# Optimization experiments

Measured on AMD Instinct MI355X. Metric: run time of the kernel, lower is better.

The kernel has to match this reference:

```python
import jax, jax.numpy as jnp
import numpy as np

N_NODES = 50000
IN_C, HID, N_CLS = 128, 128, 16
N_EDGES = 800000


def gcn_conv(x, W, b, src, dst, deg_inv_sqrt, n_nodes):
    # PyG GCNConv: h = x @ W; out[dst] += norm * h[src]; out += b
    h = x @ W                                   # [N, out_c]
    norm = deg_inv_sqrt[src] * deg_inv_sqrt[dst]  # [E]
    msgs = h[src] * norm[:, None]               # gather + scale, [E, out_c]
    out = jax.ops.segment_sum(msgs, dst, num_segments=n_nodes)
    return out + b


def setup_inputs() -> dict:
    key = jax.random.key(0)
    k1, k2, k3, k4, k5 = jax.random.split(key, 5)
    x = jax.random.normal(k1, (N_NODES, IN_C), dtype=jnp.float32)
    edge_index = jax.random.randint(k2, (2, N_EDGES), 0, N_NODES, dtype=jnp.int64)
    # glorot-ish params (torch.manual_seed(1234) in source only affects init values)
    def lin(k, fan_in, fan_out):
        s = 1.0 / np.sqrt(fan_in)
        kw, kb = jax.random.split(k)
        W = jax.random.uniform(kw, (fan_in, fan_out), minval=-s, maxval=s, dtype=jnp.float32)
        b = jax.random.uniform(kb, (fan_out,), minval=-s, maxval=s, dtype=jnp.float32)
        return W, b
    W1, b1 = lin(k3, IN_C, HID)
    W2, b2 = lin(k4, HID, HID)
    Wh, bh = lin(k5, HID, N_CLS)
    return {"x": x, "edge_index": edge_index, "W1": W1, "b1": b1,
            "W2": W2, "b2": b2, "Wh": Wh, "bh": bh}


def reference(x, edge_index, W1, b1, W2, b2, Wh, bh):
    n = x.shape[0]
    # add self-loops (PyG GCNConv default add_self_loops=True)
    loops = jnp.arange(n, dtype=edge_index.dtype)
    src = jnp.concatenate([edge_index[0], loops])
    dst = jnp.concatenate([edge_index[1], loops])
    # symmetric normalization D^{-1/2} (A+I) D^{-1/2}; degree over dst with unit weights
    deg = jax.ops.segment_sum(jnp.ones(src.shape[0], dtype=x.dtype), dst, num_segments=n)
    dis = jnp.where(deg > 0, jax.lax.rsqrt(deg), 0.0)
    h = gcn_conv(x, W1, b1, src, dst, dis, n)
    h = jax.nn.relu(h)
    h = gcn_conv(h, W2, b2, src, dst, dis, n)
    h = jax.nn.relu(h)
    return h @ Wh + bh
```

## Files before the change

### kernel.cpp

```cpp
#include <hip/hip_runtime.h>

#define CH 128
#define NCLS 16
#define CHK 16
#define NCHUNK 8
#define ECAP 131072

typedef __attribute__((ext_vector_type(8))) short bf16x8;
typedef __attribute__((ext_vector_type(4))) float f32x4;

__device__ inline ushort f2bf(float f) {
    unsigned u = __float_as_uint(f);
    unsigned r = u + 0x7fffu + ((u >> 16) & 1u);
    return (ushort)(r >> 16);
}
__device__ inline float bf2f(ushort b) {
    return __uint_as_float(((unsigned)b) << 16);
}

__global__ __launch_bounds__(256) void prep_kernel(
    const float* __restrict__ W1, const float* __restrict__ W2,
    ushort* __restrict__ w1hi, ushort* __restrict__ w1lo,
    ushort* __restrict__ w2hi, ushort* __restrict__ w2lo,
    int* __restrict__ cnt, int* __restrict__ pcnt, int* __restrict__ galloc,
    float* __restrict__ bufA, int n, int nbz) {
    int b = blockIdx.x, tid = threadIdx.x;
    if (b < 128) {
        const float* W = (b < 64) ? W1 : W2;
        ushort* Whi = (b < 64) ? w1hi : w2hi;
        ushort* Wlo = (b < 64) ? w1lo : w2lo;
        int t = ((b & 63) << 8) + tid;
        int k = t >> 7, nn = t & 127;
        float v = W[t];
        ushort h = f2bf(v);
        Whi[nn * CH + k] = h;
        Wlo[nn * CH + k] = f2bf(v - bf2f(h));
    } else if (b < 128 + nbz) {
        int i = (b - 128) * 256 + tid;
        if (i < n) cnt[i] = 0;
    } else {
        if (tid < NCHUNK * CHK) {
            int c = tid >> 4, ch = tid & 15;
            bufA[((size_t)c * (n + 1) + n) * CHK + ch] = 0.0f;
        }
        if (tid < 8) pcnt[tid] = 0;
        if (tid == 8) *galloc = 0;
    }
}

__global__ __launch_bounds__(256) void bucketcount_kernel(
    const int* __restrict__ src, const int* __restrict__ dst,
    unsigned* __restrict__ ebuf, int* __restrict__ pcnt,
    int* __restrict__ cnt, int E, float p8n) {
    __shared__ int lpos[8];
    __shared__ int lbase[8];
    int tid = threadIdx.x;
    if (tid < 8) lpos[tid] = 0;
    __syncthreads();
    int i0 = (blockIdx.x * 256 + tid) * 4;
    int part[4]; int off[4]; unsigned pk[4]; int c = 0;
    if (i0 + 3 < E) {
        int4 s4 = *(const int4*)&src[i0];
        int4 d4 = *(const int4*)&dst[i0];
        int ss[4] = {s4.x, s4.y, s4.z, s4.w};
        int dd[4] = {d4.x, d4.y, d4.z, d4.w};
        c = 4;
#pragma unroll
        for (int k = 0; k < 4; k++) {
            part[k] = min(7, (int)((float)dd[k] * p8n));
            pk[k] = ((unsigned)dd[k] << 16) | (unsigned)ss[k];
            off[k] = atomicAdd(&lpos[part[k]], 1);
            atomicAdd(&cnt[dd[k]], 1);
        }
    } else {
        for (int k = 0; k < 4 && i0 + k < E; k++) {
            int s = src[i0 + k], d = dst[i0 + k];
            part[c] = min(7, (int)((float)d * p8n));
            pk[c] = ((unsigned)d << 16) | (unsigned)s;
            off[c] = atomicAdd(&lpos[part[c]], 1);
            atomicAdd(&cnt[d], 1);
            c++;
        }
    }
    __syncthreads();
    if (tid < 8) lbase[tid] = atomicAdd(&pcnt[tid], lpos[tid]);
    __syncthreads();
    for (int k = 0; k < c; k++) {
        int idx = lbase[part[k]] + off[k];
        if (idx < ECAP) ebuf[(size_t)part[k] * ECAP + idx] = pk[k];
    }
}

__global__ __launch_bounds__(256) void place_kernel(
    const int* __restrict__ cnt, int* __restrict__ rsp,
    int* __restrict__ cursor, int* __restrict__ galloc,
    ushort* __restrict__ esrc, int n) {
    __shared__ int lds[256];
    __shared__ int gbase;
    int t = threadIdx.x;
    int i = blockIdx.x * 256 + t;
    int c = (i < n) ? cnt[i] : 0;
    int sz = (i < n) ? ((c + 8) & ~7) : 0;
    lds[t] = sz;
    __syncthreads();
    for (int off = 1; off < 256; off <<= 1) {
        int x = (t >= off) ? lds[t - off] : 0;
        __syncthreads();
        lds[t] += x;
        __syncthreads();
    }
    int incl = lds[t];
    if (t == 255) gbase = atomicAdd(galloc, incl);
    __syncthreads();
    int base = gbase + incl - sz;
    if (i < n) {
        rsp[i] = base;
        cursor[i] = base + 1;
        esrc[base] = (ushort)i;
        for (int p = base + 1 + c; p < base + sz; p++) esrc[p] = (ushort)n;
    }
}

template <bool RELU_IN>
__device__ __forceinline__ void gemm_body(
    int bx, int by, const float* __restrict__ A,
    const ushort* __restrict__ Bthi, const ushort* __restrict__ Btlo,
    const int* __restrict__ cntp, float* __restrict__ C, int n_rows) {
    const int tid = threadIdx.x;
    const int bm0 = bx * 128;
    const int wv = tid >> 6;
    const int lane = tid & 63;
    const int col = lane & 15;
    const int quad = lane >> 4;
    const int rbase = bm0 + wv * 32 + col;
    const int ntBase = by * 4;

    f32x4 acc[2][4];
#pragma unroll
    for (int m = 0; m < 2; m++)
#pragma unroll
        for (int t = 0; t < 4; t++) acc[m][t] = (f32x4){0.f, 0.f, 0.f, 0.f};

#pragma unroll
    for (int k0 = 0; k0 < 4; k0++) {
        const int kb = k0 * 32 + quad * 8;
        bf16x8 ah[2], al[2];
#pragma unroll
        for (int m = 0; m < 2; m++) {
            int arow = rbase + m * 16;
            bool av = (arow < n_rows);
            const float* __restrict__ Ap = A + (size_t)arow * CH + kb;
            float4 f0 = av ? *(const float4*)Ap       : make_float4(0.f, 0.f, 0.f, 0.f);
            float4 f1 = av ? *(const float4*)(Ap + 4) : make_float4(0.f, 0.f, 0.f, 0.f);
            if (RELU_IN) {
                f0.x = fmaxf(f0.x, 0.f); f0.y = fmaxf(f0.y, 0.f);
                f0.z = fmaxf(f0.z, 0.f); f0.w = fmaxf(f0.w, 0.f);
                f1.x = fmaxf(f1.x, 0.f); f1.y = fmaxf(f1.y, 0.f);
                f1.z = fmaxf(f1.z, 0.f); f1.w = fmaxf(f1.w, 0.f);
            }
            float fa[8] = {f0.x, f0.y, f0.z, f0.w, f1.x, f1.y, f1.z, f1.w};
#pragma unroll
            for (int j = 0; j < 8; j++) {
                ushort h = f2bf(fa[j]);
                ah[m][j] = (short)h;
                al[m][j] = (short)f2bf(fa[j] - bf2f(h));
            }
        }
#pragma unroll
        for (int t = 0; t < 4; t++) {
            const int boff = ((ntBase + t) * 16 + col) * CH + kb;
            bf16x8 bh = *(const bf16x8*)&Bthi[boff];
            bf16x8 bl = *(const bf16x8*)&Btlo[boff];
#pragma unroll
            for (int m = 0; m < 2; m++) {
                acc[m][t] = __builtin_amdgcn_mfma_f32_16x16x32_bf16(ah[m], bh, acc[m][t], 0, 0, 0);
                acc[m][t] = __builtin_amdgcn_mfma_f32_16x16x32_bf16(ah[m], bl, acc[m][t], 0, 0, 0);
                acc[m][t] = __builtin_amdgcn_mfma_f32_16x16x32_bf16(al[m], bh, acc[m][t], 0, 0, 0);
            }
        }
    }

#pragma unroll
    for (int m = 0; m < 2; m++) {
#pragma unroll
        for (int reg = 0; reg < 4; reg++) {
            int gr = bm0 + wv * 32 + m * 16 + quad * 4 + reg;
            if (gr < n_rows) {
                float d = rsqrtf((float)cntp[gr] + 1.0f);
#pragma unroll
                for (int t = 0; t < 4; t++) {
                    int nt = ntBase + t;
                    __builtin_nontemporal_store(
                        acc[m][t][reg] * d,
                        &C[((size_t)nt * (n_rows + 1) + gr) * CHK + col]);
                }
            }
        }
    }
}

template <bool RELU_IN>
__global__ __launch_bounds__(256, 4) void gemmfill_kernel(
    const float* __restrict__ A, const ushort* __restrict__ Bthi,
    const ushort* __restrict__ Btlo, const int* __restrict__ cntp,
    float* __restrict__ C, int n_rows, int nbx, int gemmBlocks,
    const unsigned* __restrict__ ebuf, const int* __restrict__ pcnt,
    int* __restrict__ cursor, ushort* __restrict__ esrc) {
    int b = blockIdx.x;
    if (b < gemmBlocks) {
        gemm_body<RELU_IN>(b % nbx, b / nbx, A, Bthi, Btlo, cntp, C, n_rows);
    } else {
        int fb = b - gemmBlocks;
        int part = fb & 7;
        int m = min(pcnt[part], ECAP);
        const unsigned* bk = ebuf + (size_t)part * ECAP;
        for (int e = (fb >> 3) * 256 + (int)threadIdx.x; e < m; e += 256 * 256) {
            unsigned pe = bk[e];
            int p = atomicAdd(&cursor[pe >> 16], 1);
            esrc[p] = (ushort)(pe & 0xffffu);
        }
    }
}

__global__ __launch_bounds__(256) void gather_kernel(
    const int* __restrict__ rsp, const int* __restrict__ cnt,
    const ushort* __restrict__ esrc, const float* __restrict__ hC,
    const float* __restrict__ bias, float* __restrict__ out, int n) {
    int c = blockIdx.x & 7;
    int wv = threadIdx.x >> 6;
    int lane = threadIdx.x & 63;
    int g = lane >> 2;
    int q = lane & 3;
    int i = (blockIdx.x >> 3) * 64 + wv * 16 + g;
    bool valid = (i < n);
    int iw = valid ? i : 0;
    const float4* __restrict__ h4 = (const float4*)(hC + (size_t)c * (n + 1) * CHK);

    float warm = 0.f;
    {
        int nblk = (n + 63) >> 6;
        size_t p = (size_t)(blockIdx.x >> 3) * 256 + threadIdx.x;
        size_t sliceF4 = ((size_t)(n + 1) * CHK) >> 2;
        for (; p < sliceF4; p += (size_t)nblk * 256) {
            float4 v = h4[p];
            warm += v.x + v.y + v.z + v.w;
        }
    }

    int beg = valid ? rsp[iw] : 0;
    int cv  = valid ? cnt[iw] : -8;
    int pc  = (cv + 8) & ~7;
    float4 acc = make_float4(0.f, 0.f, 0.f, 0.f);
    for (int j = beg; j < beg + pc; j += 8) {
        ushort4 e0 = *(const ushort4*)&esrc[j];
        ushort4 e1 = *(const ushort4*)&esrc[j + 4];
        float4 v0 = h4[(size_t)e0.x * 4 + q];
        float4 v1 = h4[(size_t)e0.y * 4 + q];
        float4 v2 = h4[(size_t)e0.z * 4 + q];
        float4 v3 = h4[(size_t)e0.w * 4 + q];
        float4 v4 = h4[(size_t)e1.x * 4 + q];
        float4 v5 = h4[(size_t)e1.y * 4 + q];
        float4 v6 = h4[(size_t)e1.z * 4 + q];
        float4 v7 = h4[(size_t)e1.w * 4 + q];
        acc.x += v0.x; acc.y += v0.y; acc.z += v0.z; acc.w += v0.w;
        acc.x += v1.x; acc.y += v1.y; acc.z += v1.z; acc.w += v1.w;
        acc.x += v2.x; acc.y += v2.y; acc.z += v2.z; acc.w += v2.w;
        acc.x += v3.x; acc.y += v3.y; acc.z += v3.z; acc.w += v3.w;
        acc.x += v4.x; acc.y += v4.y; acc.z += v4.z; acc.w += v4.w;
        acc.x += v5.x; acc.y += v5.y; acc.z += v5.z; acc.w += v5.w;
        acc.x += v6.x; acc.y += v6.y; acc.z += v6.z; acc.w += v6.w;
        acc.x += v7.x; acc.y += v7.y; acc.z += v7.z; acc.w += v7.w;
    }
    __asm__ volatile("" : : "v"(warm));
    if (valid) {
        float di = rsqrtf((float)cv + 1.0f);
        float4 bv = ((const float4*)bias)[c * 4 + q];
        f32x4 o;
        o[0] = bv.x + di * acc.x;
        o[1] = bv.y + di * acc.y;
        o[2] = bv.z + di * acc.z;
        o[3] = bv.w + di * acc.w;
        __builtin_nontemporal_store(o, (f32x4*)&((float4*)out)[(size_t)iw * 32 + c * 4 + q]);
    }
}

__global__ __launch_bounds__(256) void head_kernel(
    const float* __restrict__ A, const float* __restrict__ Wh,
    const float* __restrict__ bh, float* __restrict__ out, int n) {
    __shared__ float Ws[CH * NCLS];
    __shared__ float As[16][129];
    const int tid = threadIdx.x;
    const int n0 = blockIdx.x * 16;
#pragma unroll
    for (int i = 0; i < 8; i++) {
        int l = tid + i * 256;
        Ws[l] = Wh[l];
    }
#pragma unroll
    for (int i = 0; i < 8; i++) {
        int l = tid + i * 256;
        int r = l >> 7, c = l & 127;
        int gr = n0 + r;
        As[r][c] = (gr < n) ? fmaxf(A[(size_t)gr * CH + c], 0.0f) : 0.0f;
    }
    __syncthreads();
    int r = tid >> 4, c = tid & 15;
    float acc = bh[c];
#pragma unroll
    for (int k = 0; k < CH; k++) acc = fmaf(As[r][k], Ws[k * NCLS + c], acc);
    int gr = n0 + r;
    if (gr < n) out[(size_t)gr * NCLS + c] = acc;
}

extern "C" void kernel_launch(void* const* d_in, const int* in_sizes, int n_in,
                              void* d_out, int out_size, void* d_ws, size_t ws_size,
                              hipStream_t stream) {
    const float* x  = (const float*)d_in[0];
    const int*   ei = (const int*)d_in[1];
    const float* W1 = (const float*)d_in[2];
    const float* b1 = (const float*)d_in[3];
    const float* W2 = (const float*)d_in[4];
    const float* b2 = (const float*)d_in[5];
    const float* Wh = (const float*)d_in[6];
    const float* bh = (const float*)d_in[7];
    float* out = (float*)d_out;

    const int n = in_sizes[0] / CH;
    const int E = in_sizes[1] / 2;
    const int* src = ei;
    const int* dst = ei + E;

    ushort* w1hi = (ushort*)d_ws;
    ushort* w1lo = w1hi + CH * CH;
    ushort* w2hi = w1lo + CH * CH;
    ushort* w2lo = w2hi + CH * CH;
    float* bufA = (float*)(w2lo + CH * CH);
    float* bufB = bufA + (size_t)(n + 1) * CH;
    int* cnt    = (int*)(bufB + (size_t)n * CH);
    int* rsp    = cnt + n;
    int* cursor = rsp + n;
    int* pcnt   = cursor + n;
    int* galloc = pcnt + 8;
    ushort* esrc = (ushort*)(pcnt + 16);
    unsigned* ebuf = (unsigned*)bufB;

    const int B = 256;
    const int nbz = (n + B - 1) / B;
    const int nbx = (n + 127) / 128;
    const int gemmBlocks = nbx * 2;
    const float p8n = 8.0f / (float)n;

    prep_kernel<<<128 + nbz + 1, B, 0, stream>>>(W1, W2, w1hi, w1lo, w2hi, w2lo,
                                                 cnt, pcnt, galloc, bufA, n, nbz);
    bucketcount_kernel<<<(E + 1023) / 1024, B, 0, stream>>>(src, dst, ebuf, pcnt,
                                                            cnt, E, p8n);
    place_kernel<<<nbz, B, 0, stream>>>(cnt, rsp, cursor, galloc, esrc, n);

    const int gatherGrid = NCHUNK * ((n + 63) / 64);

    gemmfill_kernel<false><<<gemmBlocks + 2048, B, 0, stream>>>(
        x, w1hi, w1lo, cnt, bufA, n, nbx, gemmBlocks, ebuf, pcnt, cursor, esrc);
    gather_kernel<<<gatherGrid, B, 0, stream>>>(rsp, cnt, esrc, bufA, b1, bufB, n);
    gemmfill_kernel<true><<<gemmBlocks, B, 0, stream>>>(
        bufB, w2hi, w2lo, cnt, bufA, n, nbx, gemmBlocks, ebuf, pcnt, cursor, esrc);
    gather_kernel<<<gatherGrid, B, 0, stream>>>(rsp, cnt, esrc, bufA, b2, bufB, n);
    head_kernel<<<(n + 15) / 16, B, 0, stream>>>(bufB, Wh, bh, out, n);
}
```

Before: 296.4 us.

## Sort nodes by degree bin within blocks to balance gather wavefront work

The place kernel now counting-sorts the 256 nodes of each block into 16 bins by padded edge count, and writes a per-block permutation. Gather threads then process nodes in that permuted order, so nodes with similar degree share a wavefront and lanes diverge less in the edge loop. The cost is an extra LDS histogram pass in place, one more indirection load in gather, and scattered output writes.

```diff
diff --git a/kernel.cpp b/kernel.cpp
--- a/kernel.cpp
+++ b/kernel.cpp
@@ -94,26 +94,41 @@
 __global__ __launch_bounds__(256) void place_kernel(
     const int* __restrict__ cnt, int* __restrict__ rsp,
     int* __restrict__ cursor, int* __restrict__ galloc,
-    ushort* __restrict__ esrc, int n) {
-    __shared__ int lds[256];
+    ushort* __restrict__ esrc, int* __restrict__ perm, int n) {
+    __shared__ int hist[16];
+    __shared__ int histBase[16];
+    __shared__ int scanArr[256];
     __shared__ int gbase;
     int t = threadIdx.x;
     int i = blockIdx.x * 256 + t;
-    int c = (i < n) ? cnt[i] : 0;
-    int sz = (i < n) ? ((c + 8) & ~7) : 0;
-    lds[t] = sz;
+    bool valid = (i < n);
+    int c = valid ? cnt[i] : 0;
+    int sz = valid ? ((c + 8) & ~7) : 0;
+    int k = valid ? min(sz >> 3, 15) : 15;
+    if (t < 16) hist[t] = 0;
+    __syncthreads();
+    int idxInBin = atomicAdd(&hist[k], 1);
+    __syncthreads();
+    if (t == 0) {
+        int s = 0;
+#pragma unroll
+        for (int b = 0; b < 16; b++) { histBase[b] = s; s += hist[b]; }
+    }
+    __syncthreads();
+    int r = histBase[k] + idxInBin;
+    scanArr[r] = sz;
     __syncthreads();
     for (int off = 1; off < 256; off <<= 1) {
-        int x = (t >= off) ? lds[t - off] : 0;
+        int x = (t >= off) ? scanArr[t - off] : 0;
         __syncthreads();
-        lds[t] += x;
+        scanArr[t] += x;
         __syncthreads();
     }
-    int incl = lds[t];
-    if (t == 255) gbase = atomicAdd(galloc, incl);
-    __syncthreads();
-    int base = gbase + incl - sz;
-    if (i < n) {
+    if (t == 255) gbase = atomicAdd(galloc, scanArr[255]);
+    __syncthreads();
+    int base = gbase + scanArr[r] - sz;
+    perm[blockIdx.x * 256 + r] = valid ? i : n;
+    if (valid) {
         rsp[i] = base;
         cursor[i] = base + 1;
         esrc[base] = (ushort)i;
@@ -224,16 +239,18 @@
 
 __global__ __launch_bounds__(256) void gather_kernel(
     const int* __restrict__ rsp, const int* __restrict__ cnt,
-    const ushort* __restrict__ esrc, const float* __restrict__ hC,
-    const float* __restrict__ bias, float* __restrict__ out, int n) {
+    const int* __restrict__ perm, const ushort* __restrict__ esrc,
+    const float* __restrict__ hC, const float* __restrict__ bias,
+    float* __restrict__ out, int n) {
     int c = blockIdx.x & 7;
     int wv = threadIdx.x >> 6;
     int lane = threadIdx.x & 63;
     int g = lane >> 2;
     int q = lane & 3;
-    int i = (blockIdx.x >> 3) * 64 + wv * 16 + g;
-    bool valid = (i < n);
-    int iw = valid ? i : 0;
+    int slot = (blockIdx.x >> 3) * 64 + wv * 16 + g;
+    int node = perm[slot];
+    bool valid = (node < n);
+    int iw = valid ? node : 0;
     const float4* __restrict__ h4 = (const float4*)(hC + (size_t)c * (n + 1) * CHK);
 
     float warm = 0.f;
@@ -341,11 +358,12 @@
     int* cursor = rsp + n;
     int* pcnt   = cursor + n;
     int* galloc = pcnt + 8;
-    ushort* esrc = (ushort*)(pcnt + 16);
+    int* perm   = galloc + 8;
+    const int nbz = (n + 255) / 256;
+    ushort* esrc = (ushort*)(perm + nbz * 256);
     unsigned* ebuf = (unsigned*)bufB;
 
     const int B = 256;
-    const int nbz = (n + B - 1) / B;
     const int nbx = (n + 127) / 128;
     const int gemmBlocks = nbx * 2;
     const float p8n = 8.0f / (float)n;
@@ -354,15 +372,15 @@
                                                  cnt, pcnt, galloc, bufA, n, nbz);
     bucketcount_kernel<<<(E + 1023) / 1024, B, 0, stream>>>(src, dst, ebuf, pcnt,
                                                             cnt, E, p8n);
-    place_kernel<<<nbz, B, 0, stream>>>(cnt, rsp, cursor, galloc, esrc, n);
+    place_kernel<<<nbz, B, 0, stream>>>(cnt, rsp, cursor, galloc, esrc, perm, n);
 
     const int gatherGrid = NCHUNK * ((n + 63) / 64);
 
     gemmfill_kernel<false><<<gemmBlocks + 2048, B, 0, stream>>>(
         x, w1hi, w1lo, cnt, bufA, n, nbx, gemmBlocks, ebuf, pcnt, cursor, esrc);
-    gather_kernel<<<gatherGrid, B, 0, stream>>>(rsp, cnt, esrc, bufA, b1, bufB, n);
+    gather_kernel<<<gatherGrid, B, 0, stream>>>(rsp, cnt, perm, esrc, bufA, b1, bufB, n);
     gemmfill_kernel<true><<<gemmBlocks, B, 0, stream>>>(
         bufB, w2hi, w2lo, cnt, bufA, n, nbx, gemmBlocks, ebuf, pcnt, cursor, esrc);
-    gather_kernel<<<gatherGrid, B, 0, stream>>>(rsp, cnt, esrc, bufA, b2, bufB, n);
+    gather_kernel<<<gatherGrid, B, 0, stream>>>(rsp, cnt, perm, esrc, bufA, b2, bufB, n);
     head_kernel<<<(n + 15) / 16, B, 0, stream>>>(bufB, Wh, bh, out, n);
 }
```

Result: slower. 305.4 us (+3.0%).

## Stage A tile through double-buffered LDS with coalesced loads and one-time bf16 split

Applied to the files above, without the earlier changes.

The GEMM now loads each 128-row A tile cooperatively with coalesced float4 reads, converts it to hi/lo bf16 once, and stores it into a double-buffered LDS tile padded to avoid bank conflicts. The MFMA loop then reads fragments from LDS while the next k-slice is prefetched from global memory. The intent is to improve global-load coalescing and overlap loads with MFMA work. In exchange it adds barriers and about 40KB of LDS per block, and lowers the launch-bounds occupancy hint from 4 to 3 blocks.

```diff
diff --git a/kernel.cpp b/kernel.cpp
--- a/kernel.cpp
+++ b/kernel.cpp
@@ -5,6 +5,7 @@
 #define CHK 16
 #define NCHUNK 8
 #define ECAP 131072
+#define LDSK 40
 
 typedef __attribute__((ext_vector_type(8))) short bf16x8;
 typedef __attribute__((ext_vector_type(4))) float f32x4;
@@ -125,50 +126,76 @@
 __device__ __forceinline__ void gemm_body(
     int bx, int by, const float* __restrict__ A,
     const ushort* __restrict__ Bthi, const ushort* __restrict__ Btlo,
-    const int* __restrict__ cntp, float* __restrict__ C, int n_rows) {
+    const int* __restrict__ cntp, float* __restrict__ C, int n_rows,
+    ushort (*Ahi)[128 * LDSK], ushort (*Alo)[128 * LDSK]) {
     const int tid = threadIdx.x;
     const int bm0 = bx * 128;
     const int wv = tid >> 6;
     const int lane = tid & 63;
     const int col = lane & 15;
     const int quad = lane >> 4;
-    const int rbase = bm0 + wv * 32 + col;
     const int ntBase = by * 4;
 
+    int srow[4], skk[4]; bool sval[4]; const float* sptr[4];
+#pragma unroll
+    for (int i = 0; i < 4; i++) {
+        int f4 = tid + i * 256;
+        srow[i] = f4 >> 3;
+        skk[i] = (f4 & 7) * 4;
+        sval[i] = (bm0 + srow[i]) < n_rows;
+        sptr[i] = A + (size_t)(bm0 + srow[i]) * CH + skk[i];
+    }
+
     f32x4 acc[2][4];
 #pragma unroll
     for (int m = 0; m < 2; m++)
 #pragma unroll
         for (int t = 0; t < 4; t++) acc[m][t] = (f32x4){0.f, 0.f, 0.f, 0.f};
 
+    float4 ld[4];
+    auto cvtStore = [&](int bsel) {
+#pragma unroll
+        for (int i = 0; i < 4; i++) {
+            float fv[4] = {ld[i].x, ld[i].y, ld[i].z, ld[i].w};
+            ushort hs[4], ls[4];
+#pragma unroll
+            for (int j = 0; j < 4; j++) {
+                float v = RELU_IN ? fmaxf(fv[j], 0.f) : fv[j];
+                ushort h = f2bf(v);
+                hs[j] = h;
+                ls[j] = f2bf(v - bf2f(h));
+            }
+            int o = srow[i] * LDSK + skk[i];
+            *(ushort4*)&Ahi[bsel][o] = make_ushort4(hs[0], hs[1], hs[2], hs[3]);
+            *(ushort4*)&Alo[bsel][o] = make_ushort4(ls[0], ls[1], ls[2], ls[3]);
+        }
+    };
+
+#pragma unroll
+    for (int i = 0; i < 4; i++)
+        ld[i] = sval[i] ? *(const float4*)(sptr[i]) : make_float4(0.f, 0.f, 0.f, 0.f);
+    cvtStore(0);
+    __syncthreads();
+
 #pragma unroll
     for (int k0 = 0; k0 < 4; k0++) {
-        const int kb = k0 * 32 + quad * 8;
+        if (k0 < 3) {
+#pragma unroll
+            for (int i = 0; i < 4; i++)
+                ld[i] = sval[i] ? *(const float4*)(sptr[i] + (k0 + 1) * 32)
+                                : make_float4(0.f, 0.f, 0.f, 0.f);
+        }
+        const int bsel = k0 & 1;
         bf16x8 ah[2], al[2];
 #pragma unroll
         for (int m = 0; m < 2; m++) {
-            int arow = rbase + m * 16;
-            bool av = (arow < n_rows);
-            const float* __restrict__ Ap = A + (size_t)arow * CH + kb;
-            float4 f0 = av ? *(const float4*)Ap       : make_float4(0.f, 0.f, 0.f, 0.f);
-            float4 f1 = av ? *(const float4*)(Ap + 4) : make_float4(0.f, 0.f, 0.f, 0.f);
-            if (RELU_IN) {
-                f0.x = fmaxf(f0.x, 0.f); f0.y = fmaxf(f0.y, 0.f);
-                f0.z = fmaxf(f0.z, 0.f); f0.w = fmaxf(f0.w, 0.f);
-                f1.x = fmaxf(f1.x, 0.f); f1.y = fmaxf(f1.y, 0.f);
-                f1.z = fmaxf(f1.z, 0.f); f1.w = fmaxf(f1.w, 0.f);
-            }
-            float fa[8] = {f0.x, f0.y, f0.z, f0.w, f1.x, f1.y, f1.z, f1.w};
-#pragma unroll
-            for (int j = 0; j < 8; j++) {
-                ushort h = f2bf(fa[j]);
-                ah[m][j] = (short)h;
-                al[m][j] = (short)f2bf(fa[j] - bf2f(h));
-            }
+            int o = (wv * 32 + m * 16 + col) * LDSK + quad * 8;
+            ah[m] = *(bf16x8*)&Ahi[bsel][o];
+            al[m] = *(bf16x8*)&Alo[bsel][o];
         }
 #pragma unroll
         for (int t = 0; t < 4; t++) {
-            const int boff = ((ntBase + t) * 16 + col) * CH + kb;
+            const int boff = ((ntBase + t) * 16 + col) * CH + k0 * 32 + quad * 8;
             bf16x8 bh = *(const bf16x8*)&Bthi[boff];
             bf16x8 bl = *(const bf16x8*)&Btlo[boff];
 #pragma unroll
@@ -178,6 +205,8 @@
                 acc[m][t] = __builtin_amdgcn_mfma_f32_16x16x32_bf16(al[m], bh, acc[m][t], 0, 0, 0);
             }
         }
+        if (k0 < 3) cvtStore((k0 + 1) & 1);
+        __syncthreads();
     }
 
 #pragma unroll
@@ -200,15 +229,18 @@
 }
 
 template <bool RELU_IN>
-__global__ __launch_bounds__(256, 4) void gemmfill_kernel(
+__global__ __launch_bounds__(256, 3) void gemmfill_kernel(
     const float* __restrict__ A, const ushort* __restrict__ Bthi,
     const ushort* __restrict__ Btlo, const int* __restrict__ cntp,
     float* __restrict__ C, int n_rows, int nbx, int gemmBlocks,
     const unsigned* __restrict__ ebuf, const int* __restrict__ pcnt,
     int* __restrict__ cursor, ushort* __restrict__ esrc) {
+    __shared__ ushort Ahi[2][128 * LDSK];
+    __shared__ ushort Alo[2][128 * LDSK];
     int b = blockIdx.x;
     if (b < gemmBlocks) {
-        gemm_body<RELU_IN>(b % nbx, b / nbx, A, Bthi, Btlo, cntp, C, n_rows);
+        gemm_body<RELU_IN>(b % nbx, b / nbx, A, Bthi, Btlo, cntp, C, n_rows,
+                           Ahi, Alo);
     } else {
         int fb = b - gemmBlocks;
         int part = fb & 7;
```

Measured after the change: 299.3 us. No clear change (+1.0%).

## Merge prep, bucket-count and placement kernels into one persistent kernel with grid barriers

Applied to the files above, without the earlier changes.

Replaces three separate setup launches (weight split/zeroing, edge bucketing with degree counting, prefix-sum placement) with a single persistent kernel of 512 blocks. Software grid barriers built on agent-scope atomics separate the phases, and a memset resets the barrier counters before launch. The aim is to remove launch overhead and the idle gaps between the small setup kernels. In exchange it relies on all 512 blocks being co-resident, adds spin-wait barrier cost, and adds a memset call.

```diff
diff --git a/kernel.cpp b/kernel.cpp
--- a/kernel.cpp
+++ b/kernel.cpp
@@ -5,6 +5,7 @@
 #define CHK 16
 #define NCHUNK 8
 #define ECAP 131072
+#define NBLD 512
 
 typedef __attribute__((ext_vector_type(8))) short bf16x8;
 typedef __attribute__((ext_vector_type(4))) float f32x4;
@@ -18,13 +19,34 @@
     return __uint_as_float(((unsigned)b) << 16);
 }
 
-__global__ __launch_bounds__(256) void prep_kernel(
+__device__ __forceinline__ void gridbar(int* ctr, int nb) {
+    __syncthreads();
+    if (threadIdx.x == 0) {
+        __threadfence();
+        __hip_atomic_fetch_add(ctr, 1, __ATOMIC_RELEASE, __HIP_MEMORY_SCOPE_AGENT);
+        while (__hip_atomic_load(ctr, __ATOMIC_ACQUIRE, __HIP_MEMORY_SCOPE_AGENT) < nb)
+            __builtin_amdgcn_s_sleep(1);
+        __threadfence();
+    }
+    __syncthreads();
+}
+
+__global__ __launch_bounds__(256, 2) void build_kernel(
     const float* __restrict__ W1, const float* __restrict__ W2,
     ushort* __restrict__ w1hi, ushort* __restrict__ w1lo,
     ushort* __restrict__ w2hi, ushort* __restrict__ w2lo,
-    int* __restrict__ cnt, int* __restrict__ pcnt, int* __restrict__ galloc,
-    float* __restrict__ bufA, int n, int nbz) {
-    int b = blockIdx.x, tid = threadIdx.x;
+    const int* __restrict__ src, const int* __restrict__ dst,
+    unsigned* __restrict__ ebuf, int* __restrict__ pcnt,
+    int* __restrict__ cnt, int* __restrict__ rsp, int* __restrict__ cursor,
+    int* __restrict__ galloc, ushort* __restrict__ esrc,
+    float* __restrict__ bufA, int* __restrict__ bars,
+    int n, int E, float p8n, int nbz) {
+    __shared__ int lpos[8];
+    __shared__ int lbase[8];
+    __shared__ int lds[256];
+    __shared__ int gbase;
+    const int b = blockIdx.x, tid = threadIdx.x;
+
     if (b < 128) {
         const float* W = (b < 64) ? W1 : W2;
         ushort* Whi = (b < 64) ? w1hi : w2hi;
@@ -35,10 +57,9 @@
         ushort h = f2bf(v);
         Whi[nn * CH + k] = h;
         Wlo[nn * CH + k] = f2bf(v - bf2f(h));
-    } else if (b < 128 + nbz) {
-        int i = (b - 128) * 256 + tid;
-        if (i < n) cnt[i] = 0;
-    } else {
+    }
+    for (int i = b * 256 + tid; i < n; i += NBLD * 256) cnt[i] = 0;
+    if (b == 128) {
         if (tid < NCHUNK * CHK) {
             int c = tid >> 4, ch = tid & 15;
             bufA[((size_t)c * (n + 1) + n) * CHK + ch] = 0.0f;
@@ -46,78 +67,71 @@
         if (tid < 8) pcnt[tid] = 0;
         if (tid == 8) *galloc = 0;
     }
-}
-
-__global__ __launch_bounds__(256) void bucketcount_kernel(
-    const int* __restrict__ src, const int* __restrict__ dst,
-    unsigned* __restrict__ ebuf, int* __restrict__ pcnt,
-    int* __restrict__ cnt, int E, float p8n) {
-    __shared__ int lpos[8];
-    __shared__ int lbase[8];
-    int tid = threadIdx.x;
-    if (tid < 8) lpos[tid] = 0;
-    __syncthreads();
-    int i0 = (blockIdx.x * 256 + tid) * 4;
-    int part[4]; int off[4]; unsigned pk[4]; int c = 0;
-    if (i0 + 3 < E) {
-        int4 s4 = *(const int4*)&src[i0];
-        int4 d4 = *(const int4*)&dst[i0];
-        int ss[4] = {s4.x, s4.y, s4.z, s4.w};
-        int dd[4] = {d4.x, d4.y, d4.z, d4.w};
-        c = 4;
-#pragma unroll
-        for (int k = 0; k < 4; k++) {
-            part[k] = min(7, (int)((float)dd[k] * p8n));
-            pk[k] = ((unsigned)dd[k] << 16) | (unsigned)ss[k];
-            off[k] = atomicAdd(&lpos[part[k]], 1);
-            atomicAdd(&cnt[dd[k]], 1);
-        }
-    } else {
-        for (int k = 0; k < 4 && i0 + k < E; k++) {
-            int s = src[i0 + k], d = dst[i0 + k];
-            part[c] = min(7, (int)((float)d * p8n));
-            pk[c] = ((unsigned)d << 16) | (unsigned)s;
-            off[c] = atomicAdd(&lpos[part[c]], 1);
-            atomicAdd(&cnt[d], 1);
-            c++;
-        }
-    }
-    __syncthreads();
-    if (tid < 8) lbase[tid] = atomicAdd(&pcnt[tid], lpos[tid]);
-    __syncthreads();
-    for (int k = 0; k < c; k++) {
-        int idx = lbase[part[k]] + off[k];
-        if (idx < ECAP) ebuf[(size_t)part[k] * ECAP + idx] = pk[k];
-    }
-}
-
-__global__ __launch_bounds__(256) void place_kernel(
-    const int* __restrict__ cnt, int* __restrict__ rsp,
-    int* __restrict__ cursor, int* __restrict__ galloc,
-    ushort* __restrict__ esrc, int n) {
-    __shared__ int lds[256];
-    __shared__ int gbase;
-    int t = threadIdx.x;
-    int i = blockIdx.x * 256 + t;
-    int c = (i < n) ? cnt[i] : 0;
-    int sz = (i < n) ? ((c + 8) & ~7) : 0;
-    lds[t] = sz;
-    __syncthreads();
-    for (int off = 1; off < 256; off <<= 1) {
-        int x = (t >= off) ? lds[t - off] : 0;
-        __syncthreads();
-        lds[t] += x;
-        __syncthreads();
-    }
-    int incl = lds[t];
-    if (t == 255) gbase = atomicAdd(galloc, incl);
-    __syncthreads();
-    int base = gbase + incl - sz;
-    if (i < n) {
-        rsp[i] = base;
-        cursor[i] = base + 1;
-        esrc[base] = (ushort)i;
-        for (int p = base + 1 + c; p < base + sz; p++) esrc[p] = (ushort)n;
+    gridbar(&bars[0], NBLD);
+
+    const int nvb = (E + 1023) / 1024;
+    for (int vb = b; vb < nvb; vb += NBLD) {
+        if (tid < 8) lpos[tid] = 0;
+        __syncthreads();
+        int i0 = (vb * 256 + tid) * 4;
+        int part[4]; int off[4]; unsigned pk[4]; int c = 0;
+        if (i0 + 3 < E) {
+            int4 s4 = *(const int4*)&src[i0];
+            int4 d4 = *(const int4*)&dst[i0];
+            int ss[4] = {s4.x, s4.y, s4.z, s4.w};
+            int dd[4] = {d4.x, d4.y, d4.z, d4.w};
+            c = 4;
+#pragma unroll
+            for (int k = 0; k < 4; k++) {
+                part[k] = min(7, (int)((float)dd[k] * p8n));
+                pk[k] = ((unsigned)dd[k] << 16) | (unsigned)ss[k];
+                off[k] = atomicAdd(&lpos[part[k]], 1);
+                atomicAdd(&cnt[dd[k]], 1);
+            }
+        } else {
+            for (int k = 0; k < 4 && i0 + k < E; k++) {
+                int s = src[i0 + k], d = dst[i0 + k];
+                part[c] = min(7, (int)((float)d * p8n));
+                pk[c] = ((unsigned)d << 16) | (unsigned)s;
+                off[c] = atomicAdd(&lpos[part[c]], 1);
+                atomicAdd(&cnt[d], 1);
+                c++;
+            }
+        }
+        __syncthreads();
+        if (tid < 8) lbase[tid] = atomicAdd(&pcnt[tid], lpos[tid]);
+        __syncthreads();
+        for (int k = 0; k < c; k++) {
+            int idx = lbase[part[k]] + off[k];
+            if (idx < ECAP) ebuf[(size_t)part[k] * ECAP + idx] = pk[k];
+        }
+        __syncthreads();
+    }
+    gridbar(&bars[1], NBLD);
+
+    if (b < nbz) {
+        int i = b * 256 + tid;
+        int c = (i < n) ? __hip_atomic_load(&cnt[i], __ATOMIC_RELAXED,
+                                            __HIP_MEMORY_SCOPE_AGENT) : 0;
+        int sz = (i < n) ? ((c + 8) & ~7) : 0;
+        lds[tid] = sz;
+        __syncthreads();
+        for (int off = 1; off < 256; off <<= 1) {
+            int x = (tid >= off) ? lds[tid - off] : 0;
+            __syncthreads();
+            lds[tid] += x;
+            __syncthreads();
+        }
+        int incl = lds[tid];
+        if (tid == 255) gbase = atomicAdd(galloc, incl);
+        __syncthreads();
+        int base = gbase + incl - sz;
+        if (i < n) {
+            rsp[i] = base;
+            cursor[i] = base + 1;
+            esrc[base] = (ushort)i;
+            for (int p = base + 1 + c; p < base + sz; p++) esrc[p] = (ushort)n;
+        }
     }
 }
 
@@ -341,7 +355,8 @@
     int* cursor = rsp + n;
     int* pcnt   = cursor + n;
     int* galloc = pcnt + 8;
-    ushort* esrc = (ushort*)(pcnt + 16);
+    int* bars   = galloc + 8;
+    ushort* esrc = (ushort*)(bars + 8);
     unsigned* ebuf = (unsigned*)bufB;
 
     const int B = 256;
@@ -350,11 +365,10 @@
     const int gemmBlocks = nbx * 2;
     const float p8n = 8.0f / (float)n;
 
-    prep_kernel<<<128 + nbz + 1, B, 0, stream>>>(W1, W2, w1hi, w1lo, w2hi, w2lo,
-                                                 cnt, pcnt, galloc, bufA, n, nbz);
-    bucketcount_kernel<<<(E + 1023) / 1024, B, 0, stream>>>(src, dst, ebuf, pcnt,
-                                                            cnt, E, p8n);
-    place_kernel<<<nbz, B, 0, stream>>>(cnt, rsp, cursor, galloc, esrc, n);
+    hipMemsetAsync(bars, 0, 16, stream);
+    build_kernel<<<NBLD, B, 0, stream>>>(W1, W2, w1hi, w1lo, w2hi, w2lo,
+                                         src, dst, ebuf, pcnt, cnt, rsp, cursor,
+                                         galloc, esrc, bufA, bars, n, E, p8n, nbz);
 
     const int gatherGrid = NCHUNK * ((n + 63) / 64);
 
```

Measured after the change: 448.9 us. +51.4%, slower.
